# Optimization experiments

Hardware: AMD Instinct MI355X
Metric: run time of the kernel (lower is better)

## Reference

```python
import jax, jax.numpy as jnp
import numpy as np

K_PRE_NMS = 2000      # number of top-scoring candidates fed to NMS
IOU_THRESHOLD = 0.5
IMAGE_SIZE = 800.0


def decode_boxes(deltas, locations, stride):
    """Faithful fcos_apply_deltas_to_locations (incl. the all(-1) special case
    and the swapped-y-coordinate convention of the source)."""
    d = deltas * stride
    x, y = locations[:, 0], locations[:, 1]
    boxes = jnp.stack([x - d[:, 0], y - d[:, 1], x + d[:, 2], y + d[:, 3]], axis=1)
    all_bg = jnp.all(deltas == -1)
    degen = jnp.stack([x, y, x, y], axis=1)
    return jnp.where(all_bg, degen, boxes)


def nms_keep_mask(boxes_sorted, iou_threshold):
    """Sequential NMS on score-descending-sorted boxes. Reproduces the source's
    exact (quirky) IoU math: y1=boxes[:,3], y2=boxes[:,1], w/h via abs().
    Returns bool keep mask aligned with the sorted order."""
    K = boxes_sorted.shape[0]
    x1, y1 = boxes_sorted[:, 0], boxes_sorted[:, 3]
    x2, y2 = boxes_sorted[:, 2], boxes_sorted[:, 1]
    area = (x2 - x1) * (y2 - y1)
    idx = jnp.arange(K)

    def body(i, state):
        active, keep = state
        is_kept = active[i]
        keep = keep.at[i].set(is_kept)
        xx1 = jnp.maximum(x1[i], x1)
        yy1 = jnp.minimum(y1[i], y1)
        xx2 = jnp.minimum(x2[i], x2)
        yy2 = jnp.maximum(y2[i], y2)
        inter = jnp.abs(xx2 - xx1) * jnp.abs(yy2 - yy1)
        iou = inter / (area[i] + area - inter)
        suppress = is_kept & (iou > iou_threshold) & (idx > i)
        return active & ~suppress, keep

    active0 = jnp.ones((K,), dtype=bool)
    keep0 = jnp.zeros((K,), dtype=bool)
    _, keep = jax.lax.fori_loop(0, K, body, (active0, keep0))
    return keep


def setup_inputs() -> dict:
    key = jax.random.key(0)
    k1, k2, k3 = jax.random.split(key, 3)
    N, C = 1048576, 20
    deltas = jax.random.normal(k1, (N, 4), dtype=jnp.float32) * 4.0 + 8.0
    locations = jax.random.uniform(k2, (N, 2), dtype=jnp.float32) * IMAGE_SIZE
    logits = jax.random.normal(k3, (N, C), dtype=jnp.float32)
    return {"deltas": deltas, "locations": locations, "logits": logits, "stride": 8}


def reference(deltas, locations, logits, stride):
    # 1) box delta decode (all N locations)
    boxes = decode_boxes(deltas, locations, stride)
    # 2) per-location best class score / class id
    probs = jax.nn.sigmoid(logits)              # [N, C]
    cls_scores = jnp.max(probs, axis=1)         # [N]
    class_ids = jnp.argmax(probs, axis=1)       # [N]
    # 3) pre-NMS top-k
    top_scores, top_idx = jax.lax.top_k(cls_scores, K_PRE_NMS)
    cand_boxes = boxes[top_idx]                 # [K, 4]
    cand_cls = class_ids[top_idx]               # [K]
    # 4) class-offset trick (class_spec_nms)
    max_coord = jnp.max(cand_boxes)
    offsets = cand_cls.astype(cand_boxes.dtype) * (max_coord + 1.0)
    boxes_for_nms = cand_boxes + offsets[:, None]
    # 5) sort by score descending (top_k already sorted; argsort is faithful to nms())
    order = jnp.argsort(-top_scores)
    keep = nms_keep_mask(boxes_for_nms[order], IOU_THRESHOLD)
    return cand_boxes[order], top_scores[order], cand_cls[order], keep
```

## Files before the change

### kernel.cpp

```cpp
#include <hip/hip_runtime.h>
#include <stdint.h>
#include <math.h>

#pragma clang fp contract(off)

#define N_ROWS 1048576
#define N_CLS  20
#define K_TOP  2000
#define CAND_MAX 4096
#define H_COPIES 4
#define MAGIC 0x5AD0C0DEu
#define NBLK_SCORE 512

#define SC_CNT   0
#define SC_MAXK  1
#define SC_DONE  2
#define SC_BAR   3
#define SC_FLAG  4

static constexpr size_t OFF_MKEY  = 0;
static constexpr size_t OFF_CLS   = OFF_MKEY + 4ull * N_ROWS;
static constexpr size_t OFF_HIST1 = OFF_CLS + (size_t)N_ROWS;
static constexpr size_t OFF_HIST2 = OFF_HIST1 + 4096;
static constexpr size_t OFF_SCAL  = OFF_HIST2 + 4096;
static constexpr size_t OFF_GRP   = OFF_SCAL + 64;
static constexpr size_t OFF_ZIN   = OFF_GRP + 256;
static constexpr size_t OFF_CAND  = OFF_ZIN + 256;
static constexpr size_t OFF_MASK  = OFF_CAND + 8ull * CAND_MAX;

__device__ __forceinline__ uint32_t mono_key(float f) {
    uint32_t u = __float_as_uint(f);
    return u ^ ((u & 0x80000000u) ? 0xFFFFFFFFu : 0x80000000u);
}
__device__ __forceinline__ float mono_inv(uint32_t k) {
    uint32_t u = (k & 0x80000000u) ? (k ^ 0x80000000u) : ~k;
    return __uint_as_float(u);
}

__global__ __launch_bounds__(256, 4) void k_score(const float* __restrict__ logits,
                                                  uint32_t* __restrict__ mkey,
                                                  uint8_t* __restrict__ cls,
                                                  uint32_t* __restrict__ hist1,
                                                  uint32_t* __restrict__ hist2,
                                                  uint32_t* __restrict__ scal,
                                                  uint32_t* __restrict__ zin) {
    __shared__ uint32_t stage[256 * 21];
    __shared__ uint32_t h1[256];
    __shared__ uint32_t sfx[256];
    __shared__ uint32_t sb0;
    int t = threadIdx.x, b = blockIdx.x;

    if (b < 8) {
        uint32_t zd = atomicExch(&hist1[b * 256 + t], 0u);
        if (b == 7 && t < 80) zd += atomicExch(&hist1[2048 + t], 0u);
        asm volatile("" :: "v"(zd));
        asm volatile("s_waitcnt vmcnt(0)" ::: "memory");
        __syncthreads();
        if (t == 0) atomicExch(&zin[b], MAGIC);
    }

    h1[t] = 0;
    __syncthreads();
    size_t rowbase0 = (size_t)b * 2048;
    for (int g = 0; g < 8; ++g) {
        const float4* src = (const float4*)(logits + (rowbase0 + (size_t)g * 256) * N_CLS);
#pragma unroll
        for (int q = 0; q < 5; ++q) {
            float4 v = src[q * 256 + t];
            int w0 = (q * 256 + t) * 4;
#pragma unroll
            for (int e = 0; e < 4; ++e) {
                int w = w0 + e;
                stage[w + ((w * 52429u) >> 20)] = __float_as_uint((&v.x)[e]);
            }
        }
        __syncthreads();
        const uint32_t* row = &stage[t * 21];
        float m = __uint_as_float(row[0]); int ci = 0;
#pragma unroll
        for (int c = 1; c < 20; ++c) {
            float v = __uint_as_float(row[c]);
            if (v > m) { m = v; ci = c; }
        }
        size_t ri = rowbase0 + (size_t)g * 256 + t;
        uint32_t u = mono_key(m);
        mkey[ri] = u;
        cls[ri] = (uint8_t)ci;
        atomicAdd(&h1[u >> 24], 1u);
        __syncthreads();
    }

    for (;;) {
        int ok = 1;
        if (t < 8) ok = (atomicAdd(&zin[t], 0u) == MAGIC) ? 1 : 0;
        if (__syncthreads_count(ok) == 256) break;
        __builtin_amdgcn_s_sleep(16);
    }

    uint32_t hv = h1[t], dm = 0;
    if (hv) dm = atomicAdd(&hist1[(b & 3) * 256 + t], hv);
    asm volatile("" :: "v"(dm));
    asm volatile("s_waitcnt vmcnt(0)" ::: "memory");
    __syncthreads();
    if (t == 0) {
        uint32_t old = atomicAdd(&scal[SC_BAR], 1u);
        if (old == (uint32_t)(NBLK_SCORE - 1)) atomicExch(&scal[SC_FLAG], MAGIC);
    }
    for (;;) {
        int ok = 1;
        if (t == 0) ok = (atomicAdd(&scal[SC_FLAG], 0u) == MAGIC) ? 1 : 0;
        if (__syncthreads_count(ok) == 256) break;
        __builtin_amdgcn_s_sleep(64);
    }

    uint32_t hh = 0;
#pragma unroll
    for (int k = 0; k < H_COPIES; ++k) hh += atomicAdd(&hist1[k * 256 + t], 0u);
    sfx[t] = hh;
    __syncthreads();
    for (int off = 1; off < 256; off <<= 1) {
        uint32_t v = (t + off < 256) ? sfx[t + off] : 0;
        __syncthreads();
        sfx[t] += v;
        __syncthreads();
    }
    if (sfx[t] >= (uint32_t)K_TOP && (t == 255 || sfx[t + 1] < (uint32_t)K_TOP)) sb0 = (uint32_t)t;
    __syncthreads();
    uint32_t b0 = sb0;

    h1[t] = 0;
    __syncthreads();
    for (int g = 0; g < 8; ++g) {
        uint32_t u = mkey[rowbase0 + (size_t)g * 256 + t];
        if ((u >> 24) == b0) atomicAdd(&h1[(u >> 16) & 0xFFu], 1u);
    }
    __syncthreads();
    hv = h1[t];
    if (hv) atomicAdd(&hist2[(b & 3) * 256 + t], hv);
}

__device__ __forceinline__ void find8(const uint32_t* __restrict__ hist1,
                                      uint32_t* sfx, uint32_t* pb0, uint32_t* pR1,
                                      uint32_t& b0, uint32_t& R1) {
    int t = threadIdx.x;
    uint32_t h = 0;
#pragma unroll
    for (int k = 0; k < H_COPIES; ++k) h += hist1[k * 256 + t];
    sfx[t] = h;
    __syncthreads();
    for (int off = 1; off < 256; off <<= 1) {
        uint32_t v = (t + off < 256) ? sfx[t + off] : 0;
        __syncthreads();
        sfx[t] += v;
        __syncthreads();
    }
    if (sfx[t] >= (uint32_t)K_TOP && (t == 255 || sfx[t + 1] < (uint32_t)K_TOP)) {
        *pb0 = (uint32_t)t;
        *pR1 = (uint32_t)K_TOP - (sfx[t] - h);
    }
    __syncthreads();
    b0 = *pb0; R1 = *pR1;
}

__global__ __launch_bounds__(256) void k_compact(const uint32_t* __restrict__ mkey,
                                                 const uint32_t* __restrict__ hist1,
                                                 const uint32_t* __restrict__ hist2,
                                                 uint32_t* __restrict__ scal,
                                                 unsigned long long* __restrict__ cand) {
    __shared__ uint32_t sfx[256];
    __shared__ uint32_t sb0, sR1, sT;
    __shared__ uint32_t cnt, gbase;
    __shared__ uint64_t stg[1024];
    int t = threadIdx.x;
    int lane = t & 63;
    if (t == 0) cnt = 0;
    uint32_t b0, R1;
    find8(hist1, sfx, &sb0, &sR1, b0, R1);
    uint32_t h = 0;
#pragma unroll
    for (int k = 0; k < H_COPIES; ++k) h += hist2[k * 256 + t];
    __syncthreads();
    sfx[t] = h;
    __syncthreads();
    for (int off = 1; off < 256; off <<= 1) {
        uint32_t v = (t + off < 256) ? sfx[t + off] : 0;
        __syncthreads();
        sfx[t] += v;
        __syncthreads();
    }
    if (sfx[t] >= R1 && (t == 255 || sfx[t + 1] < R1)) {
        uint32_t t16 = (b0 << 8) | (uint32_t)t;
        sT = (t16 > 0) ? (t16 - 1) : 0;
    }
    __syncthreads();
    uint32_t T = sT;
    const uint4* m4 = (const uint4*)mkey;
    size_t base = (size_t)blockIdx.x * 1024;
    for (int it = 0; it < 4; ++it) {
        uint32_t r0 = (uint32_t)((base + it * 256 + t) * 4);
        uint4 v = m4[base + it * 256 + t];
#pragma unroll
        for (int e = 0; e < 4; ++e) {
            uint32_t u = (e == 0) ? v.x : (e == 1) ? v.y : (e == 2) ? v.z : v.w;
            bool pass = (u >> 16) >= T;
            unsigned long long bal = __ballot(pass);
            if (bal) {
                uint32_t wbase = 0;
                if (lane == 0) wbase = atomicAdd(&cnt, (uint32_t)__popcll(bal));
                wbase = __shfl(wbase, 0);
                if (pass) {
                    uint32_t pos = wbase + (uint32_t)__popcll(bal & ((1ull << lane) - 1ull));
                    if (pos < 1024) stg[pos] = ((uint64_t)u << 32) | (r0 + e);
                }
            }
        }
    }
    __syncthreads();
    uint32_t n = cnt; if (n > 1024) n = 1024;
    if (t == 0 && n) gbase = atomicAdd(&scal[SC_CNT], n);
    __syncthreads();
    if (n) {
        uint32_t gb = gbase;
        for (uint32_t i = t; i < n; i += 256) {
            uint32_t pos = gb + i;
            if (pos < (uint32_t)CAND_MAX) cand[pos] = stg[i];
        }
    }
}

__global__ __launch_bounds__(256) void k_rank(const unsigned long long* __restrict__ cand,
                                              uint32_t* __restrict__ scal,
                                              const float* __restrict__ deltas,
                                              const float* __restrict__ locs,
                                              const int* __restrict__ stridep,
                                              const uint8_t* __restrict__ cls,
                                              float* __restrict__ out) {
    __shared__ uint64_t keys[CAND_MAX];
    int t = threadIdx.x;
    uint32_t M = scal[SC_CNT];
    if (M > (uint32_t)CAND_MAX) M = CAND_MAX;
    for (uint32_t i = t; i < M; i += 256) {
        unsigned long long cd = cand[i];
        uint32_t mk = (uint32_t)(cd >> 32);
        uint32_t row = (uint32_t)cd & (N_ROWS - 1);
        float m = mono_inv(mk);
        float ef = (float)exp(-(double)m);
        float s = 1.0f / (1.0f + ef);
        keys[i] = ((uint64_t)(~__float_as_uint(s)) << 32) | row;
    }
    __syncthreads();
    int wid = t >> 6, lane = t & 63;
    float stridef = (float)(*stridep);
    float wmx = -3.4e38f;
    for (uint32_t c = (uint32_t)blockIdx.x * 4 + wid; c < M; c += 256) {
        uint64_t myk = keys[c];
        uint32_t r = 0;
        for (uint32_t j = lane; j < M; j += 64) r += (keys[j] < myk) ? 1u : 0u;
#pragma unroll
        for (int o = 32; o > 0; o >>= 1) r += __shfl_down(r, o);
        if (lane == 0 && r < (uint32_t)K_TOP) {
            uint32_t row = (uint32_t)myk & (N_ROWS - 1);
            float s = __uint_as_float(~(uint32_t)(myk >> 32));
            float4 dl = ((const float4*)deltas)[row];
            float2 lc = ((const float2*)locs)[row];
            float d0 = dl.x * stridef, d1 = dl.y * stridef, d2 = dl.z * stridef, d3 = dl.w * stridef;
            float b0f = lc.x - d0, b1f = lc.y - d1, b2f = lc.x + d2, b3f = lc.y + d3;
            float4 bx = { b0f, b1f, b2f, b3f };
            *(float4*)&out[4 * r] = bx;
            out[8000 + r] = s;
            out[10000 + r] = (float)cls[row];
            wmx = fmaxf(wmx, fmaxf(fmaxf(b0f, b1f), fmaxf(b2f, b3f)));
        }
    }
    if (lane == 0) atomicMax(&scal[SC_MAXK], mono_key(wmx));
}

__global__ __launch_bounds__(256) void k_maskscan(const float* __restrict__ out_ro,
                                                  uint32_t* __restrict__ scal,
                                                  uint64_t* __restrict__ mask,
                                                  unsigned long long* __restrict__ grp,
                                                  uint32_t* __restrict__ zin,
                                                  float* __restrict__ out) {
    __shared__ int lastdone;
    int t = threadIdx.x;
    int lane = t & 63;
    int i = blockIdx.x * 4 + (t >> 6);
    float off1 = mono_inv(scal[SC_MAXK]) + 1.0f;
    float4 boxi = *(const float4*)&out_ro[4 * i];
    float oi = out_ro[10000 + i] * off1;
    float x1i = boxi.x + oi, y2i = boxi.y + oi, x2i = boxi.z + oi, y1i = boxi.w + oi;
    float ai = (x2i - x1i) * (y2i - y1i);
    unsigned long long dummy = 0;
    for (int jb = 0; jb < 32; ++jb) {
        int j = jb * 64 + lane;
        bool sup = false;
        if (j < K_TOP && j > i) {
            float4 boxj = *(const float4*)&out_ro[4 * j];
            float oj = out_ro[10000 + j] * off1;
            float x1j = boxj.x + oj, y2j = boxj.y + oj, x2j = boxj.z + oj, y1j = boxj.w + oj;
            float aj = (x2j - x1j) * (y2j - y1j);
            float xx1 = fmaxf(x1i, x1j);
            float yy1 = fminf(y1i, y1j);
            float xx2 = fminf(x2i, x2j);
            float yy2 = fmaxf(y2i, y2j);
            float inter = fabsf(xx2 - xx1) * fabsf(yy2 - yy1);
            float iou = inter / ((ai + aj) - inter);
            sup = iou > 0.5f;
        }
        unsigned long long bits = __ballot(sup);
        if (lane == 0) {
            dummy += atomicExch(&mask[(size_t)i * 32 + jb], bits);
            if (bits) dummy += atomicOr(&grp[i >> 6], 1ull << (i & 63));
        }
    }
    asm volatile("" :: "v"(dummy));
    asm volatile("s_waitcnt vmcnt(0) lgkmcnt(0)" ::: "memory");
    __syncthreads();
    if (t == 0) {
        unsigned old = atomicAdd(&scal[SC_DONE], 1u);
        lastdone = (old == (unsigned)(gridDim.x - 1)) ? 1 : 0;
    }
    __syncthreads();
    if (!lastdone) return;

    if (t < 64) {
        int l = t;
        uint64_t g = (l < 32) ? atomicOr(&grp[l], 0ull) : 0ull;
        uint64_t active = ~0ull;
        if (__ballot(g != 0ull)) {
            for (int gg = 0; gg < 32; ++gg) {
                uint64_t nz = __shfl(g, gg);
                while (nz) {
                    int b = __ffsll((long long)nz) - 1;
                    nz &= nz - 1;
                    int ii = gg * 64 + b;
                    uint64_t aw = __shfl(active, gg);
                    bool kept = (aw >> b) & 1ull;
                    uint64_t m = (l < 32) ? atomicOr(&mask[(size_t)ii * 32 + l], 0ull) : 0ull;
                    if (kept) active &= ~m;
                }
            }
        }
        if (l < 32) {
            int limit = K_TOP - l * 64;
            int nvec = limit < 64 ? limit / 4 : 16;
            for (int v = 0; v < nvec; ++v) {
                float4 f;
                f.x = ((active >> (4 * v + 0)) & 1ull) ? 1.0f : 0.0f;
                f.y = ((active >> (4 * v + 1)) & 1ull) ? 1.0f : 0.0f;
                f.z = ((active >> (4 * v + 2)) & 1ull) ? 1.0f : 0.0f;
                f.w = ((active >> (4 * v + 3)) & 1ull) ? 1.0f : 0.0f;
                *(float4*)&out[12000 + l * 64 + 4 * v] = f;
            }
        }
    }
    if (t < 8) atomicExch(&zin[t], 0u);
}

extern "C" void kernel_launch(void* const* d_in, const int* in_sizes, int n_in,
                              void* d_out, int out_size, void* d_ws, size_t ws_size,
                              hipStream_t stream) {
    const float* deltas = (const float*)d_in[0];
    const float* locs   = (const float*)d_in[1];
    const float* logits = (const float*)d_in[2];
    const int*   stridep = (const int*)d_in[3];
    float* out = (float*)d_out;
    char* ws = (char*)d_ws;

    uint32_t* mkey  = (uint32_t*)(ws + OFF_MKEY);
    uint8_t*  cls   = (uint8_t*)(ws + OFF_CLS);
    uint32_t* hist1 = (uint32_t*)(ws + OFF_HIST1);
    uint32_t* hist2 = (uint32_t*)(ws + OFF_HIST2);
    uint32_t* scal  = (uint32_t*)(ws + OFF_SCAL);
    unsigned long long* grp = (unsigned long long*)(ws + OFF_GRP);
    uint32_t* zin   = (uint32_t*)(ws + OFF_ZIN);
    unsigned long long* cand = (unsigned long long*)(ws + OFF_CAND);
    uint64_t* mask  = (uint64_t*)(ws + OFF_MASK);

    k_score<<<dim3(NBLK_SCORE), dim3(256), 0, stream>>>(logits, mkey, cls, hist1, hist2, scal, zin);
    k_compact<<<dim3(256), dim3(256), 0, stream>>>(mkey, hist1, hist2, scal, cand);
    k_rank<<<dim3(64), dim3(256), 0, stream>>>(cand, scal, deltas, locs, stridep, cls, out);
    k_maskscan<<<dim3(500), dim3(256), 0, stream>>>(out, scal, mask, grp, zin, out);
}
```

Before: 97.90 us.

## Replace in-kernel grid barrier with separate second-level histogram kernel

The software grid-wide barrier (atomic counter plus spin on a flag) inside k_score is removed, along with the second histogram pass that followed it. That pass moves into a new k_hist2 kernel, which recomputes the top byte bucket from hist1 and scans mkey with uint4 loads. k_score now launches 1024 blocks of 1024 rows each instead of 512 blocks of 2048 rows, and drops the occupancy hint. This removes spin-wait latency and any reliance on all blocks being co-resident, at the cost of one extra kernel launch and a second full read of mkey.

```diff
diff --git a/kernel.cpp b/kernel.cpp
--- a/kernel.cpp
+++ b/kernel.cpp
@@ -10,13 +10,10 @@
 #define CAND_MAX 4096
 #define H_COPIES 4
 #define MAGIC 0x5AD0C0DEu
-#define NBLK_SCORE 512
 
 #define SC_CNT   0
 #define SC_MAXK  1
 #define SC_DONE  2
-#define SC_BAR   3
-#define SC_FLAG  4
 
 static constexpr size_t OFF_MKEY  = 0;
 static constexpr size_t OFF_CLS   = OFF_MKEY + 4ull * N_ROWS;
@@ -37,17 +34,13 @@
     return __uint_as_float(u);
 }
 
-__global__ __launch_bounds__(256, 4) void k_score(const float* __restrict__ logits,
-                                                  uint32_t* __restrict__ mkey,
-                                                  uint8_t* __restrict__ cls,
-                                                  uint32_t* __restrict__ hist1,
-                                                  uint32_t* __restrict__ hist2,
-                                                  uint32_t* __restrict__ scal,
-                                                  uint32_t* __restrict__ zin) {
+__global__ __launch_bounds__(256) void k_score(const float* __restrict__ logits,
+                                               uint32_t* __restrict__ mkey,
+                                               uint8_t* __restrict__ cls,
+                                               uint32_t* __restrict__ hist1,
+                                               uint32_t* __restrict__ zin) {
     __shared__ uint32_t stage[256 * 21];
     __shared__ uint32_t h1[256];
-    __shared__ uint32_t sfx[256];
-    __shared__ uint32_t sb0;
     int t = threadIdx.x, b = blockIdx.x;
 
     if (b < 8) {
@@ -61,8 +54,8 @@
 
     h1[t] = 0;
     __syncthreads();
-    size_t rowbase0 = (size_t)b * 2048;
-    for (int g = 0; g < 8; ++g) {
+    size_t rowbase0 = (size_t)b * 1024;
+    for (int g = 0; g < 4; ++g) {
         const float4* src = (const float4*)(logits + (rowbase0 + (size_t)g * 256) * N_CLS);
 #pragma unroll
         for (int q = 0; q < 5; ++q) {
@@ -96,47 +89,8 @@
         if (__syncthreads_count(ok) == 256) break;
         __builtin_amdgcn_s_sleep(16);
     }
-
-    uint32_t hv = h1[t], dm = 0;
-    if (hv) dm = atomicAdd(&hist1[(b & 3) * 256 + t], hv);
-    asm volatile("" :: "v"(dm));
-    asm volatile("s_waitcnt vmcnt(0)" ::: "memory");
-    __syncthreads();
-    if (t == 0) {
-        uint32_t old = atomicAdd(&scal[SC_BAR], 1u);
-        if (old == (uint32_t)(NBLK_SCORE - 1)) atomicExch(&scal[SC_FLAG], MAGIC);
-    }
-    for (;;) {
-        int ok = 1;
-        if (t == 0) ok = (atomicAdd(&scal[SC_FLAG], 0u) == MAGIC) ? 1 : 0;
-        if (__syncthreads_count(ok) == 256) break;
-        __builtin_amdgcn_s_sleep(64);
-    }
-
-    uint32_t hh = 0;
-#pragma unroll
-    for (int k = 0; k < H_COPIES; ++k) hh += atomicAdd(&hist1[k * 256 + t], 0u);
-    sfx[t] = hh;
-    __syncthreads();
-    for (int off = 1; off < 256; off <<= 1) {
-        uint32_t v = (t + off < 256) ? sfx[t + off] : 0;
-        __syncthreads();
-        sfx[t] += v;
-        __syncthreads();
-    }
-    if (sfx[t] >= (uint32_t)K_TOP && (t == 255 || sfx[t + 1] < (uint32_t)K_TOP)) sb0 = (uint32_t)t;
-    __syncthreads();
-    uint32_t b0 = sb0;
-
-    h1[t] = 0;
-    __syncthreads();
-    for (int g = 0; g < 8; ++g) {
-        uint32_t u = mkey[rowbase0 + (size_t)g * 256 + t];
-        if ((u >> 24) == b0) atomicAdd(&h1[(u >> 16) & 0xFFu], 1u);
-    }
-    __syncthreads();
-    hv = h1[t];
-    if (hv) atomicAdd(&hist2[(b & 3) * 256 + t], hv);
+    uint32_t hv = h1[t];
+    if (hv) atomicAdd(&hist1[(b & 3) * 256 + t], hv);
 }
 
 __device__ __forceinline__ void find8(const uint32_t* __restrict__ hist1,
@@ -160,6 +114,26 @@
     }
     __syncthreads();
     b0 = *pb0; R1 = *pR1;
+}
+
+__global__ __launch_bounds__(256) void k_hist2(const uint32_t* __restrict__ mkey,
+                                               const uint32_t* __restrict__ hist1,
+                                               uint32_t* __restrict__ hist2) {
+    __shared__ uint32_t sfx[256];
+    __shared__ uint32_t h2[256];
+    __shared__ uint32_t sb0, sR1;
+    int t = threadIdx.x;
+    h2[t] = 0;
+    uint32_t b0, R1;
+    find8(hist1, sfx, &sb0, &sR1, b0, R1);
+    uint4 v = ((const uint4*)mkey)[(size_t)blockIdx.x * 256 + t];
+    if ((v.x >> 24) == b0) atomicAdd(&h2[(v.x >> 16) & 0xFFu], 1u);
+    if ((v.y >> 24) == b0) atomicAdd(&h2[(v.y >> 16) & 0xFFu], 1u);
+    if ((v.z >> 24) == b0) atomicAdd(&h2[(v.z >> 16) & 0xFFu], 1u);
+    if ((v.w >> 24) == b0) atomicAdd(&h2[(v.w >> 16) & 0xFFu], 1u);
+    __syncthreads();
+    uint32_t hv = h2[t];
+    if (hv) atomicAdd(&hist2[(blockIdx.x & (H_COPIES - 1)) * 256 + t], hv);
 }
 
 __global__ __launch_bounds__(256) void k_compact(const uint32_t* __restrict__ mkey,
@@ -377,7 +351,8 @@
     unsigned long long* cand = (unsigned long long*)(ws + OFF_CAND);
     uint64_t* mask  = (uint64_t*)(ws + OFF_MASK);
 
-    k_score<<<dim3(NBLK_SCORE), dim3(256), 0, stream>>>(logits, mkey, cls, hist1, hist2, scal, zin);
+    k_score<<<dim3(1024), dim3(256), 0, stream>>>(logits, mkey, cls, hist1, zin);
+    k_hist2<<<dim3(1024), dim3(256), 0, stream>>>(mkey, hist1, hist2);
     k_compact<<<dim3(256), dim3(256), 0, stream>>>(mkey, hist1, hist2, scal, cand);
     k_rank<<<dim3(64), dim3(256), 0, stream>>>(cand, scal, deltas, locs, stridep, cls, out);
     k_maskscan<<<dim3(500), dim3(256), 0, stream>>>(out, scal, mask, grp, zin, out);
```

New measurement: 87.36 us. 1.12x faster.
